# Performance work log

Hardware: AMD Instinct MI355X
Metric: run time of the kernel (lower is better)

## Reference

```python
import jax, jax.numpy as jnp
import numpy as np
from jax import lax

EPS = 1e-4
THRESHOLD = 0.0


@jax.custom_vjp
def ternary(x):
    return jnp.where(x <= -THRESHOLD, -1.0,
                     jnp.where(x >= THRESHOLD, 1.0, 0.0)).astype(x.dtype)


def _ternary_fwd(x):
    return ternary(x), x


def _ternary_bwd(x, g):
    # STE: pass gradient where -1 < x < 1, zero where |x| >= 1
    mask = (x < 1.0) & (x > -1.0)
    return (g * mask.astype(g.dtype),)


ternary.defvjp(_ternary_fwd, _ternary_bwd)


def setup_inputs() -> dict:
    key = jax.random.key(0)
    k1, k2, k3 = jax.random.split(key, 3)
    N, C_in, H, W = 32, 256, 56, 56
    C_out, K = 256, 3
    x = jax.random.normal(k1, (N, C_in, H, W), dtype=jnp.float32)
    gamma = jnp.ones((C_in,), dtype=jnp.float32)
    beta = jnp.zeros((C_in,), dtype=jnp.float32)
    fan_in = C_in * K * K
    weight = jax.random.normal(k2, (C_out, C_in, K, K), dtype=jnp.float32) / np.sqrt(fan_in)
    bias = jax.random.normal(k3, (C_out,), dtype=jnp.float32) * 0.01
    return {"x": x, "gamma": gamma, "beta": beta, "weight": weight, "bias": bias}


def reference(x, gamma, beta, weight, bias):
    # BatchNorm2d (training mode: batch statistics, biased var), eps=1e-4
    mean = jnp.mean(x, axis=(0, 2, 3), keepdims=True)
    var = jnp.mean(jnp.square(x - mean), axis=(0, 2, 3), keepdims=True)
    xn = (x - mean) * lax.rsqrt(var + EPS)
    xn = xn * gamma[None, :, None, None] + beta[None, :, None, None]
    # Ternarize to {-1, 0, 1}
    t = ternary(xn)
    # Conv2d stride=1, padding=1 (NCHW / OIHW)
    y = lax.conv_general_dilated(
        t, weight, window_strides=(1, 1), padding=[(1, 1), (1, 1)],
        dimension_numbers=("NCHW", "OIHW", "NCHW"))
    y = y + bias[None, :, None, None]
    return jax.nn.relu(y)
```

## Files before the change

kernel.cpp:

```cpp
#include <hip/hip_runtime.h>
#include <stdint.h>

#define NN 32
#define CI 256
#define CO 256
#define HH 56
#define WW 56
#define TPH 58
#define TPW 72
#define CNT (NN*HH*WW)

typedef int i32x4 __attribute__((ext_vector_type(4)));

__device__ __forceinline__ void gld16(const void* g, void* l) {
    __builtin_amdgcn_global_load_lds(
        (const __attribute__((address_space(1))) void*)(uintptr_t)g,
        (__attribute__((address_space(3))) void*)(uint32_t)(uintptr_t)l,
        16, 0, 0);
}

__global__ void stats_part(const float* __restrict__ x, double* __restrict__ part) {
    const int c = blockIdx.x, sp = blockIdx.y;
    double s = 0.0, ss = 0.0;
    const size_t base = ((size_t)(sp * 4) * CI + c) * 3136;
    for (int idx = threadIdx.x; idx < 4 * 784; idx += 256) {
        int nl = idx / 784, q = idx % 784;
        const float4 v = *(const float4*)(x + base + (size_t)nl * CI * 3136 + q * 4);
        double a = v.x, b = v.y, cc = v.z, d = v.w;
        s  += (a + b) + (cc + d);
        ss += (a * a + b * b) + (cc * cc + d * d);
    }
    for (int off = 32; off > 0; off >>= 1) {
        s  += __shfl_down(s, off, 64);
        ss += __shfl_down(ss, off, 64);
    }
    __shared__ double red[8];
    int wid = threadIdx.x >> 6, lane = threadIdx.x & 63;
    if (lane == 0) { red[wid] = s; red[4 + wid] = ss; }
    __syncthreads();
    if (threadIdx.x == 0) {
        part[(sp * 256 + c) * 2]     = (red[0] + red[1]) + (red[2] + red[3]);
        part[(sp * 256 + c) * 2 + 1] = (red[4] + red[5]) + (red[6] + red[7]);
    }
}

__global__ void stats_final(const double* __restrict__ part,
                            const float* __restrict__ gamma,
                            const float* __restrict__ beta,
                            double* __restrict__ stats) {
    const int c = threadIdx.x;
    double S = 0.0, SS = 0.0;
    for (int sp = 0; sp < 8; ++sp) {
        S  += part[(sp * 256 + c) * 2];
        SS += part[(sp * 256 + c) * 2 + 1];
    }
    double mean = S / (double)CNT;
    double var  = SS / (double)CNT - mean * mean;
    double invstd = 1.0 / sqrt(var + 1e-4);
    double scale = (double)gamma[c] * invstd;
    double shift = (double)beta[c] - mean * scale;
    stats[2 * c]     = scale;
    stats[2 * c + 1] = shift;
}

__global__ void wtrans_kernel(const float* __restrict__ w,
                              int8_t* __restrict__ wT,
                              float* __restrict__ qscale) {
    const int co = blockIdx.x;
    const float* wp = w + (size_t)co * 2304;
    float v[9], m = 0.f;
#pragma unroll
    for (int it = 0; it < 9; ++it) {
        v[it] = wp[threadIdx.x + it * 256];
        m = fmaxf(m, fabsf(v[it]));
    }
    for (int off = 32; off > 0; off >>= 1) m = fmaxf(m, __shfl_down(m, off, 64));
    __shared__ float red[4];
    __shared__ float qsh;
    int wid = threadIdx.x >> 6, lane = threadIdx.x & 63;
    if (lane == 0) red[wid] = m;
    __syncthreads();
    if (threadIdx.x == 0) {
        float mx = fmaxf(fmaxf(red[0], red[1]), fmaxf(red[2], red[3]));
        float q = (mx > 0.f) ? mx / 127.f : 1.f;
        qsh = q;
        qscale[co] = q;
    }
    __syncthreads();
    const float q = qsh;
#pragma unroll
    for (int it = 0; it < 9; ++it) {
        int idx = threadIdx.x + it * 256;
        int ci = idx / 9, tap = idx % 9;
        int chunk = ci >> 6, cis = ci & 63;
        int iq = __float2int_rn(v[it] / q);
        iq = iq > 127 ? 127 : (iq < -127 ? -127 : iq);
        wT[((size_t)(tap * 4 + chunk) * 256 + co) * 64 + cis] = (int8_t)iq;
    }
}

__global__ void halo_kernel(int8_t* __restrict__ tp) {
    const int b = blockIdx.x, n = b >> 1, r = (b & 1) * 57;
    i32x4* dst = (i32x4*)(tp + ((size_t)n * TPH + r) * TPW * CI);
    const i32x4 z = {0, 0, 0, 0};
    for (int p = threadIdx.x; p < TPW * CI / 16; p += 256) dst[p] = z;
}

__global__ void ternarize_kernel(const float* __restrict__ x,
                                 const double* __restrict__ stats,
                                 int8_t* __restrict__ tp) {
    const int h = blockIdx.x, n = blockIdx.y;
    __shared__ int8_t L[56 * 260];
    const size_t xb = ((size_t)n * CI) * 3136 + (size_t)h * 56;
    for (int idx = threadIdx.x; idx < CI * 56; idx += 256) {
        int ci = idx / 56, w = idx - ci * 56;
        float val = x[xb + (size_t)ci * 3136 + w];
        double sc = stats[2 * ci], sh = stats[2 * ci + 1];
        L[w * 260 + ci] = (fma(sc, (double)val, sh) > 0.0) ? (int8_t)1 : (int8_t)-1;
    }
    __syncthreads();
    i32x4* rowp = (i32x4*)(tp + ((size_t)n * TPH + h + 1) * TPW * CI);
    for (int p = threadIdx.x; p < TPW * 16; p += 256) {
        int wo = p >> 4, c16 = p & 15;
        i32x4 v = {0, 0, 0, 0};
        if (wo >= 1 && wo <= 56) {
            const int* lp = (const int*)&L[(wo - 1) * 260 + c16 * 16];
            v.x = lp[0]; v.y = lp[1]; v.z = lp[2]; v.w = lp[3];
        }
        rowp[p] = v;
    }
}

__device__ __forceinline__ void stage_chunk(const int8_t* __restrict__ g0,
                                            int8_t* lbuf, int chunk, int tid) {
#pragma unroll
    for (int j = 0; j < 5; ++j) {
        int p = tid + j * 256;
        if (j < 4 || tid < 128) {
            int row = p / 288, rem = p - row * 288;
            int wp = rem >> 2, s = rem & 3;
            int g = (s - wp) & 3;
            gld16(g0 + (size_t)row * TPW * CI + wp * 256 + chunk * 64 + g * 16,
                  lbuf + p * 16);
        }
    }
}

__launch_bounds__(256, 2)
__global__ void conv_kernel(const int8_t* __restrict__ wT,
                            const int8_t* __restrict__ tp,
                            const float* __restrict__ bias,
                            const float* __restrict__ qscale,
                            float* __restrict__ out) {
    const int co_t = blockIdx.x;
    const int h0   = blockIdx.y * 2;
    const int n    = blockIdx.z;
    const int tid  = threadIdx.x;
    const int lane = tid & 63, wid = tid >> 6;
    const int l15 = lane & 15, qd = lane >> 4;
    const int m_off = (wid & 1) * 64;
    const int rowsel = wid >> 1;

    __shared__ int8_t Bsh[2 * 4 * TPW * 64];

    i32x4 acc[4][4];
#pragma unroll
    for (int i = 0; i < 4; ++i)
#pragma unroll
        for (int j = 0; j < 4; ++j) acc[i][j] = (i32x4){0, 0, 0, 0};

    const int8_t* g0 = tp + ((size_t)n * TPH + h0) * TPW * CI;

    stage_chunk(g0, Bsh, 0, tid);
    for (int c = 0; c < 4; ++c) {
        __syncthreads();
        if (c < 3) stage_chunk(g0, Bsh + ((c + 1) & 1) * 18432, c + 1, tid);
        const int8_t* lb = Bsh + (c & 1) * 18432;
#pragma unroll
        for (int kh = 0; kh < 3; ++kh) {
            const int brow = (rowsel + kh) * TPW;
#pragma unroll
            for (int kw = 0; kw < 3; ++kw) {
                const int tap = kh * 3 + kw;
                const i32x4* ap = (const i32x4*)(wT +
                    ((size_t)(tap * 4 + c) * 256 + co_t * 128 + m_off) * 64);
                i32x4 a[4], b[4];
#pragma unroll
                for (int i = 0; i < 4; ++i)
                    a[i] = ap[(i * 16 + l15) * 4 + qd];
#pragma unroll
                for (int j = 0; j < 4; ++j) {
                    int wp = j * 16 + l15 + kw;
                    int slot = (qd + wp) & 3;
                    b[j] = *(const i32x4*)&lb[(brow + wp) * 64 + slot * 16];
                }
#pragma unroll
                for (int i = 0; i < 4; ++i)
#pragma unroll
                    for (int j = 0; j < 4; ++j)
                        acc[i][j] = __builtin_amdgcn_mfma_i32_16x16x64_i8(
                            a[i], b[j], acc[i][j], 0, 0, 0);
            }
        }
    }

    const int h_out = h0 + rowsel;
#pragma unroll
    for (int i = 0; i < 4; ++i) {
        const int co = co_t * 128 + m_off + i * 16 + qd * 4;
        const float4 bv = *(const float4*)&bias[co];
        const float4 qv = *(const float4*)&qscale[co];
        const float bb[4] = {bv.x, bv.y, bv.z, bv.w};
        const float qq[4] = {qv.x, qv.y, qv.z, qv.w};
#pragma unroll
        for (int j = 0; j < 4; ++j) {
            const int w = j * 16 + l15;
            if (w < 56) {
                const size_t ob = (((size_t)n * CO + co) * HH + h_out) * WW + w;
#pragma unroll
                for (int r = 0; r < 4; ++r) {
                    float v = (float)acc[i][j][r] * qq[r] + bb[r];
                    out[ob + (size_t)r * (HH * WW)] = v > 0.f ? v : 0.f;
                }
            }
        }
    }
}

extern "C" void kernel_launch(void* const* d_in, const int* in_sizes, int n_in,
                              void* d_out, int out_size, void* d_ws, size_t ws_size,
                              hipStream_t stream) {
    const float* x      = (const float*)d_in[0];
    const float* gamma  = (const float*)d_in[1];
    const float* beta   = (const float*)d_in[2];
    const float* weight = (const float*)d_in[3];
    const float* bias   = (const float*)d_in[4];
    float* out = (float*)d_out;

    double* part    = (double*)d_ws;
    double* stats   = (double*)((char*)d_ws + 32768);
    float*  qscale  = (float*) ((char*)d_ws + 36864);
    int8_t* wT      = (int8_t*)((char*)d_ws + 65536);
    int8_t* tp      = (int8_t*)((char*)d_ws + 1048576);

    wtrans_kernel<<<256, 256, 0, stream>>>(weight, wT, qscale);
    halo_kernel<<<64, 256, 0, stream>>>(tp);
    stats_part<<<dim3(256, 8), 256, 0, stream>>>(x, part);
    stats_final<<<1, 256, 0, stream>>>(part, gamma, beta, stats);
    ternarize_kernel<<<dim3(HH, NN), 256, 0, stream>>>(x, stats, tp);
    conv_kernel<<<dim3(2, 28, NN), 256, 0, stream>>>(wT, tp, bias, qscale, out);
}
```

Baseline: 327.1 us.

## Fuse prep kernels, split ternary activations into per-chunk planes, preload weights per chunk

Merges the weight quantisation and partial batch-stat kernels into one launch, and folds stats finalisation and halo zeroing into the ternarize kernel, which now reads x with float4 loads. Cuts launch count from six to three. The padded ternary tensor is stored as four channel-chunk planes, so each conv stage reads contiguous 64-byte pixels. The conv kernel loads all 9 taps of int8 weights into registers once per chunk instead of per tap. This raises register pressure (36 extra vector registers of weights) under launch bounds of 2 blocks per SIMD, and every ternarize block recomputes the stats.

```diff
diff --git a/kernel.cpp b/kernel.cpp
--- a/kernel.cpp
+++ b/kernel.cpp
@@ -19,120 +19,127 @@
         16, 0, 0);
 }
 
-__global__ void stats_part(const float* __restrict__ x, double* __restrict__ part) {
-    const int c = blockIdx.x, sp = blockIdx.y;
-    double s = 0.0, ss = 0.0;
-    const size_t base = ((size_t)(sp * 4) * CI + c) * 3136;
-    for (int idx = threadIdx.x; idx < 4 * 784; idx += 256) {
-        int nl = idx / 784, q = idx % 784;
-        const float4 v = *(const float4*)(x + base + (size_t)nl * CI * 3136 + q * 4);
-        double a = v.x, b = v.y, cc = v.z, d = v.w;
-        s  += (a + b) + (cc + d);
-        ss += (a * a + b * b) + (cc * cc + d * d);
-    }
-    for (int off = 32; off > 0; off >>= 1) {
-        s  += __shfl_down(s, off, 64);
-        ss += __shfl_down(ss, off, 64);
-    }
-    __shared__ double red[8];
-    int wid = threadIdx.x >> 6, lane = threadIdx.x & 63;
-    if (lane == 0) { red[wid] = s; red[4 + wid] = ss; }
+__global__ void prep_kernel(const float* __restrict__ x,
+                            const float* __restrict__ w,
+                            double* __restrict__ part,
+                            int8_t* __restrict__ wT,
+                            float* __restrict__ qscale) {
+    __shared__ double dred[8];
+    __shared__ float fred[4];
+    __shared__ float qsh;
+    const int wid = threadIdx.x >> 6, lane = threadIdx.x & 63;
+
+    if (blockIdx.y < 8) {
+        const int c = blockIdx.x, sp = blockIdx.y;
+        double s = 0.0, ss = 0.0;
+        const size_t base = ((size_t)(sp * 4) * CI + c) * 3136;
+        for (int idx = threadIdx.x; idx < 4 * 784; idx += 256) {
+            int nl = idx / 784, q = idx % 784;
+            const float4 v = *(const float4*)(x + base + (size_t)nl * CI * 3136 + q * 4);
+            double a = v.x, b = v.y, cc = v.z, d = v.w;
+            s  += (a + b) + (cc + d);
+            ss += (a * a + b * b) + (cc * cc + d * d);
+        }
+        for (int off = 32; off > 0; off >>= 1) {
+            s  += __shfl_down(s, off, 64);
+            ss += __shfl_down(ss, off, 64);
+        }
+        if (lane == 0) { dred[wid] = s; dred[4 + wid] = ss; }
+        __syncthreads();
+        if (threadIdx.x == 0) {
+            part[(sp * 256 + c) * 2]     = (dred[0] + dred[1]) + (dred[2] + dred[3]);
+            part[(sp * 256 + c) * 2 + 1] = (dred[4] + dred[5]) + (dred[6] + dred[7]);
+        }
+    } else {
+        const int co = blockIdx.x;
+        const float* wp = w + (size_t)co * 2304;
+        float v[9], m = 0.f;
+#pragma unroll
+        for (int it = 0; it < 9; ++it) {
+            v[it] = wp[threadIdx.x + it * 256];
+            m = fmaxf(m, fabsf(v[it]));
+        }
+        for (int off = 32; off > 0; off >>= 1) m = fmaxf(m, __shfl_down(m, off, 64));
+        if (lane == 0) fred[wid] = m;
+        __syncthreads();
+        if (threadIdx.x == 0) {
+            float mx = fmaxf(fmaxf(fred[0], fred[1]), fmaxf(fred[2], fred[3]));
+            float q = (mx > 0.f) ? mx / 127.f : 1.f;
+            qsh = q;
+            qscale[co] = q;
+        }
+        __syncthreads();
+        const float q = qsh;
+#pragma unroll
+        for (int it = 0; it < 9; ++it) {
+            int idx = threadIdx.x + it * 256;
+            int ci = idx / 9, tap = idx % 9;
+            int chunk = ci >> 6, cis = ci & 63;
+            int iq = __float2int_rn(v[it] / q);
+            iq = iq > 127 ? 127 : (iq < -127 ? -127 : iq);
+            wT[((size_t)(tap * 4 + chunk) * 256 + co) * 64 + cis] = (int8_t)iq;
+        }
+    }
+}
+
+__global__ void ternarize_kernel(const float* __restrict__ x,
+                                 const double* __restrict__ part,
+                                 const float* __restrict__ gamma,
+                                 const float* __restrict__ beta,
+                                 int8_t* __restrict__ tp) {
+    __shared__ double scs[256], shs[256];
+    __shared__ int8_t L[56 * 272];
+    const int hp = blockIdx.x, n = blockIdx.y;
+    const int tid = threadIdx.x;
+
+    {
+        const int c = tid;
+        double S = 0.0, SS = 0.0;
+#pragma unroll
+        for (int sp = 0; sp < 8; ++sp) {
+            S  += part[(sp * 256 + c) * 2];
+            SS += part[(sp * 256 + c) * 2 + 1];
+        }
+        double mean = S / (double)CNT;
+        double var  = SS / (double)CNT - mean * mean;
+        double invstd = 1.0 / sqrt(var + 1e-4);
+        double scale = (double)gamma[c] * invstd;
+        scs[c] = scale;
+        shs[c] = (double)beta[c] - mean * scale;
+    }
     __syncthreads();
-    if (threadIdx.x == 0) {
-        part[(sp * 256 + c) * 2]     = (red[0] + red[1]) + (red[2] + red[3]);
-        part[(sp * 256 + c) * 2 + 1] = (red[4] + red[5]) + (red[6] + red[7]);
-    }
-}
-
-__global__ void stats_final(const double* __restrict__ part,
-                            const float* __restrict__ gamma,
-                            const float* __restrict__ beta,
-                            double* __restrict__ stats) {
-    const int c = threadIdx.x;
-    double S = 0.0, SS = 0.0;
-    for (int sp = 0; sp < 8; ++sp) {
-        S  += part[(sp * 256 + c) * 2];
-        SS += part[(sp * 256 + c) * 2 + 1];
-    }
-    double mean = S / (double)CNT;
-    double var  = SS / (double)CNT - mean * mean;
-    double invstd = 1.0 / sqrt(var + 1e-4);
-    double scale = (double)gamma[c] * invstd;
-    double shift = (double)beta[c] - mean * scale;
-    stats[2 * c]     = scale;
-    stats[2 * c + 1] = shift;
-}
-
-__global__ void wtrans_kernel(const float* __restrict__ w,
-                              int8_t* __restrict__ wT,
-                              float* __restrict__ qscale) {
-    const int co = blockIdx.x;
-    const float* wp = w + (size_t)co * 2304;
-    float v[9], m = 0.f;
-#pragma unroll
-    for (int it = 0; it < 9; ++it) {
-        v[it] = wp[threadIdx.x + it * 256];
-        m = fmaxf(m, fabsf(v[it]));
-    }
-    for (int off = 32; off > 0; off >>= 1) m = fmaxf(m, __shfl_down(m, off, 64));
-    __shared__ float red[4];
-    __shared__ float qsh;
-    int wid = threadIdx.x >> 6, lane = threadIdx.x & 63;
-    if (lane == 0) red[wid] = m;
+
+    const bool interior = (hp >= 1 && hp <= 56);
+    if (interior) {
+        const int h = hp - 1;
+        const size_t xb = ((size_t)n * CI) * 3136 + (size_t)h * 56;
+        for (int idx = tid; idx < CI * 14; idx += 256) {
+            int ci = idx / 14, wq = idx - ci * 14;
+            const float4 v = *(const float4*)(x + xb + (size_t)ci * 3136 + wq * 4);
+            double sc = scs[ci], sh = shs[ci];
+            L[(wq * 4 + 0) * 272 + ci] = (fma(sc, (double)v.x, sh) > 0.0) ? (int8_t)1 : (int8_t)-1;
+            L[(wq * 4 + 1) * 272 + ci] = (fma(sc, (double)v.y, sh) > 0.0) ? (int8_t)1 : (int8_t)-1;
+            L[(wq * 4 + 2) * 272 + ci] = (fma(sc, (double)v.z, sh) > 0.0) ? (int8_t)1 : (int8_t)-1;
+            L[(wq * 4 + 3) * 272 + ci] = (fma(sc, (double)v.w, sh) > 0.0) ? (int8_t)1 : (int8_t)-1;
+        }
+    }
     __syncthreads();
-    if (threadIdx.x == 0) {
-        float mx = fmaxf(fmaxf(red[0], red[1]), fmaxf(red[2], red[3]));
-        float q = (mx > 0.f) ? mx / 127.f : 1.f;
-        qsh = q;
-        qscale[co] = q;
-    }
-    __syncthreads();
-    const float q = qsh;
-#pragma unroll
-    for (int it = 0; it < 9; ++it) {
-        int idx = threadIdx.x + it * 256;
-        int ci = idx / 9, tap = idx % 9;
-        int chunk = ci >> 6, cis = ci & 63;
-        int iq = __float2int_rn(v[it] / q);
-        iq = iq > 127 ? 127 : (iq < -127 ? -127 : iq);
-        wT[((size_t)(tap * 4 + chunk) * 256 + co) * 64 + cis] = (int8_t)iq;
-    }
-}
-
-__global__ void halo_kernel(int8_t* __restrict__ tp) {
-    const int b = blockIdx.x, n = b >> 1, r = (b & 1) * 57;
-    i32x4* dst = (i32x4*)(tp + ((size_t)n * TPH + r) * TPW * CI);
-    const i32x4 z = {0, 0, 0, 0};
-    for (int p = threadIdx.x; p < TPW * CI / 16; p += 256) dst[p] = z;
-}
-
-__global__ void ternarize_kernel(const float* __restrict__ x,
-                                 const double* __restrict__ stats,
-                                 int8_t* __restrict__ tp) {
-    const int h = blockIdx.x, n = blockIdx.y;
-    __shared__ int8_t L[56 * 260];
-    const size_t xb = ((size_t)n * CI) * 3136 + (size_t)h * 56;
-    for (int idx = threadIdx.x; idx < CI * 56; idx += 256) {
-        int ci = idx / 56, w = idx - ci * 56;
-        float val = x[xb + (size_t)ci * 3136 + w];
-        double sc = stats[2 * ci], sh = stats[2 * ci + 1];
-        L[w * 260 + ci] = (fma(sc, (double)val, sh) > 0.0) ? (int8_t)1 : (int8_t)-1;
-    }
-    __syncthreads();
-    i32x4* rowp = (i32x4*)(tp + ((size_t)n * TPH + h + 1) * TPW * CI);
-    for (int p = threadIdx.x; p < TPW * 16; p += 256) {
+
+    const size_t planeN = (size_t)NN * TPH * TPW * 64;
+    for (int p = tid; p < TPW * 16; p += 256) {
         int wo = p >> 4, c16 = p & 15;
+        int chunk = c16 >> 2, ci16 = c16 & 3;
         i32x4 v = {0, 0, 0, 0};
-        if (wo >= 1 && wo <= 56) {
-            const int* lp = (const int*)&L[(wo - 1) * 260 + c16 * 16];
-            v.x = lp[0]; v.y = lp[1]; v.z = lp[2]; v.w = lp[3];
-        }
-        rowp[p] = v;
-    }
-}
-
-__device__ __forceinline__ void stage_chunk(const int8_t* __restrict__ g0,
-                                            int8_t* lbuf, int chunk, int tid) {
+        if (interior && wo >= 1 && wo <= 56)
+            v = *(const i32x4*)&L[(wo - 1) * 272 + c16 * 16];
+        int8_t* dst = tp + chunk * planeN +
+                      (((size_t)n * TPH + hp) * TPW + wo) * 64 + ci16 * 16;
+        *(i32x4*)dst = v;
+    }
+}
+
+__device__ __forceinline__ void stage_chunk(const int8_t* __restrict__ gc,
+                                            int8_t* lbuf, int tid) {
 #pragma unroll
     for (int j = 0; j < 5; ++j) {
         int p = tid + j * 256;
@@ -140,8 +147,7 @@
             int row = p / 288, rem = p - row * 288;
             int wp = rem >> 2, s = rem & 3;
             int g = (s - wp) & 3;
-            gld16(g0 + (size_t)row * TPW * CI + wp * 256 + chunk * 64 + g * 16,
-                  lbuf + p * 16);
+            gld16(gc + (row * TPW + wp) * 64 + g * 16, lbuf + p * 16);
         }
     }
 }
@@ -160,6 +166,7 @@
     const int l15 = lane & 15, qd = lane >> 4;
     const int m_off = (wid & 1) * 64;
     const int rowsel = wid >> 1;
+    const int cobase = co_t * 128 + m_off;
 
     __shared__ int8_t Bsh[2 * 4 * TPW * 64];
 
@@ -169,12 +176,23 @@
 #pragma unroll
         for (int j = 0; j < 4; ++j) acc[i][j] = (i32x4){0, 0, 0, 0};
 
-    const int8_t* g0 = tp + ((size_t)n * TPH + h0) * TPW * CI;
-
-    stage_chunk(g0, Bsh, 0, tid);
+    const size_t planeN = (size_t)NN * TPH * TPW * 64;
+    const int8_t* g0 = tp + (((size_t)n * TPH + h0) * TPW) * 64;
+    const i32x4* wbT = (const i32x4*)wT;
+
+    stage_chunk(g0, Bsh, tid);
+#pragma unroll
     for (int c = 0; c < 4; ++c) {
         __syncthreads();
-        if (c < 3) stage_chunk(g0, Bsh + ((c + 1) & 1) * 18432, c + 1, tid);
+        i32x4 aw[9][4];
+#pragma unroll
+        for (int t = 0; t < 9; ++t)
+#pragma unroll
+            for (int i = 0; i < 4; ++i)
+                aw[t][i] = wbT[((size_t)((t * 4 + c) * 256) + cobase + i * 16 + l15) * 4 + qd];
+        __builtin_amdgcn_sched_barrier(0);
+        if (c < 3) stage_chunk(g0 + (size_t)(c + 1) * planeN,
+                               Bsh + ((c + 1) & 1) * 18432, tid);
         const int8_t* lb = Bsh + (c & 1) * 18432;
 #pragma unroll
         for (int kh = 0; kh < 3; ++kh) {
@@ -182,12 +200,7 @@
 #pragma unroll
             for (int kw = 0; kw < 3; ++kw) {
                 const int tap = kh * 3 + kw;
-                const i32x4* ap = (const i32x4*)(wT +
-                    ((size_t)(tap * 4 + c) * 256 + co_t * 128 + m_off) * 64);
-                i32x4 a[4], b[4];
-#pragma unroll
-                for (int i = 0; i < 4; ++i)
-                    a[i] = ap[(i * 16 + l15) * 4 + qd];
+                i32x4 b[4];
 #pragma unroll
                 for (int j = 0; j < 4; ++j) {
                     int wp = j * 16 + l15 + kw;
@@ -199,7 +212,7 @@
 #pragma unroll
                     for (int j = 0; j < 4; ++j)
                         acc[i][j] = __builtin_amdgcn_mfma_i32_16x16x64_i8(
-                            a[i], b[j], acc[i][j], 0, 0, 0);
+                            aw[tap][i], b[j], acc[i][j], 0, 0, 0);
             }
         }
     }
@@ -207,7 +220,7 @@
     const int h_out = h0 + rowsel;
 #pragma unroll
     for (int i = 0; i < 4; ++i) {
-        const int co = co_t * 128 + m_off + i * 16 + qd * 4;
+        const int co = cobase + i * 16 + qd * 4;
         const float4 bv = *(const float4*)&bias[co];
         const float4 qv = *(const float4*)&qscale[co];
         const float bb[4] = {bv.x, bv.y, bv.z, bv.w};
@@ -238,15 +251,11 @@
     float* out = (float*)d_out;
 
     double* part    = (double*)d_ws;
-    double* stats   = (double*)((char*)d_ws + 32768);
-    float*  qscale  = (float*) ((char*)d_ws + 36864);
+    float*  qscale  = (float*) ((char*)d_ws + 32768);
     int8_t* wT      = (int8_t*)((char*)d_ws + 65536);
     int8_t* tp      = (int8_t*)((char*)d_ws + 1048576);
 
-    wtrans_kernel<<<256, 256, 0, stream>>>(weight, wT, qscale);
-    halo_kernel<<<64, 256, 0, stream>>>(tp);
-    stats_part<<<dim3(256, 8), 256, 0, stream>>>(x, part);
-    stats_final<<<1, 256, 0, stream>>>(part, gamma, beta, stats);
-    ternarize_kernel<<<dim3(HH, NN), 256, 0, stream>>>(x, stats, tp);
+    prep_kernel<<<dim3(256, 9), 256, 0, stream>>>(x, weight, part, wT, qscale);
+    ternarize_kernel<<<dim3(TPH, NN), 256, 0, stream>>>(x, part, gamma, beta, tp);
     conv_kernel<<<dim3(2, 28, NN), 256, 0, stream>>>(wT, tp, bias, qscale, out);
 }
```

New measurement: 347.5 us. 1.06x slower.
